# Kernel tuning notes

Measured on AMD Instinct MI355X. Metric: run time of the kernel, lower is better.

The kernel has to match this reference:

```python
import jax, jax.numpy as jnp
import numpy as np

B, T, D_MODEL, HEAD = 4, 4096, 1024, 64

def setup_inputs() -> dict:
    key = jax.random.key(0)
    ks = jax.random.split(key, 7)
    s = 0.02  # typical init scale
    return {
        "x":  jax.random.normal(ks[0], (B, T, D_MODEL), dtype=jnp.float32),
        "Wq": jax.random.normal(ks[1], (D_MODEL, HEAD), dtype=jnp.float32) * s,
        "bq": jnp.zeros((HEAD,), dtype=jnp.float32),
        "Wk": jax.random.normal(ks[2], (D_MODEL, HEAD), dtype=jnp.float32) * s,
        "bk": jnp.zeros((HEAD,), dtype=jnp.float32),
        "Wv": jax.random.normal(ks[3], (D_MODEL, HEAD), dtype=jnp.float32) * s,
        "bv": jnp.zeros((HEAD,), dtype=jnp.float32),
    }

def reference(x, Wq, bq, Wk, bk, Wv, bv):
    Bz, Tz, C = x.shape
    q = x @ Wq + bq                      # (B,T,H)
    k = x @ Wk + bk                      # (B,T,H)
    v = x @ Wv + bv                      # (B,T,H)
    # NOTE: original scales by sqrt(C) = sqrt(d_model), not sqrt(head_size)
    att = jnp.einsum("bth,bsh->bts", q, k) / jnp.sqrt(jnp.float32(C))
    causal = jnp.tril(jnp.ones((Tz, Tz), dtype=bool))
    att = jnp.where(causal, att, -jnp.inf)
    att = jax.nn.softmax(att, axis=-1)
    return jnp.einsum("bts,bsh->bth", att, v)  # (B,T,H)
```

## Files before the change

kernel.cpp:

```cpp
#include <hip/hip_runtime.h>
#include <hip/hip_bf16.h>
#include <hip/hip_fp16.h>

#define T_SEQ 4096
#define DMODEL 1024
#define HEAD 64
#define NBATCH 4
#define NSEG 544
#define S2LOG 0.04508422f

typedef __attribute__((ext_vector_type(8))) short bf16x8;
typedef __attribute__((ext_vector_type(4))) float f32x4;

__device__ __forceinline__ unsigned short f2bf(float f) {
    unsigned int b = __float_as_uint(f);
    unsigned int r = b + 0x7FFFu + ((b >> 16) & 1u);
    return (unsigned short)(r >> 16);
}
__device__ __forceinline__ unsigned int pk_bf16(float a, float b) {
    __hip_bfloat162 h = __float22bfloat162_rn(make_float2(a, b));
    unsigned int u; __builtin_memcpy(&u, &h, 4); return u;
}
__device__ __forceinline__ void dma16(const void* g, void* s) {
    __builtin_amdgcn_global_load_lds(
        (const __attribute__((address_space(1))) unsigned int*)g,
        (__attribute__((address_space(3))) unsigned int*)s, 16, 0, 0);
}

__global__ __launch_bounds__(256) void prep_w(
    const float* __restrict__ Wq, const float* __restrict__ Wk,
    const float* __restrict__ Wv, unsigned short* __restrict__ Wtb)
{
    __shared__ unsigned short tl[64 * 72];
    const int bid = blockIdx.x;
    const int m   = bid >> 4;
    const int k0  = (bid & 15) * 64;
    const float* W = (m == 0) ? Wq : (m == 1) ? Wk : Wv;
    const int t  = threadIdx.x;
    const int kr = t >> 2, qtr = t & 3;
#pragma unroll
    for (int i = 0; i < 4; ++i) {
        float4 wv4 = *(const float4*)&W[(k0 + kr) * 64 + qtr * 16 + i * 4];
        tl[(qtr * 16 + i * 4 + 0) * 72 + kr] = f2bf(wv4.x);
        tl[(qtr * 16 + i * 4 + 1) * 72 + kr] = f2bf(wv4.y);
        tl[(qtr * 16 + i * 4 + 2) * 72 + kr] = f2bf(wv4.z);
        tl[(qtr * 16 + i * 4 + 3) * 72 + kr] = f2bf(wv4.w);
    }
    __syncthreads();
#pragma unroll
    for (int c = 0; c < 2; ++c) {
        const int lin = c * 256 + t;
        const int n = lin >> 3, k8 = lin & 7;
        const int k = k0 + k8 * 8;
        const int sg = k >> 7, koff = k & 127;
        *(uint4*)&Wtb[((long)(sg * 192 + m * 64 + n)) * 128 + koff] =
            *(const uint4*)&tl[n * 72 + k8 * 8];
    }
}

__global__ __launch_bounds__(512, 2) void qkv_mfma(
    const float* __restrict__ x, const unsigned short* __restrict__ Wtb,
    const float* __restrict__ bq, const float* __restrict__ bk,
    const float* __restrict__ bv,
    unsigned short* __restrict__ qo, unsigned short* __restrict__ ko,
    unsigned short* __restrict__ vt)
{
    __shared__ __align__(16) unsigned short xs[2][8192];
    __shared__ __align__(16) unsigned short wsd[2][24576];
    const int t    = threadIdx.x;
    const int lane = t & 63;
    const int l15  = lane & 15, quad = lane >> 4;
    const int wv   = __builtin_amdgcn_readfirstlane(t >> 6);
    const int rowg = wv >> 2;
    const int colg = wv & 3;
    const long row0 = (long)blockIdx.x * 64;

    float bias[3];
#pragma unroll
    for (int ntl = 0; ntl < 3; ++ntl) {
        const int c = colg * 48 + ntl * 16 + l15;
        bias[ntl] = (c < 64) ? bq[c] : (c < 128) ? bk[c - 64] : bv[c - 128];
    }
    f32x4 acc[2][3];
#pragma unroll
    for (int mt = 0; mt < 2; ++mt)
#pragma unroll
        for (int ntl = 0; ntl < 3; ++ntl)
            acc[mt][ntl] = (f32x4){bias[ntl], bias[ntl], bias[ntl], bias[ntl]};

    float4 g[4];
    auto load_stage = [&](int sg) {
#pragma unroll
        for (int s = 0; s < 4; ++s) {
            const int id = s * 512 + t, row = id >> 5, off = id & 31;
            g[s] = *(const float4*)&x[(row0 + row) * DMODEL + sg * 128 + off * 4];
        }
    };
    auto write_stage = [&](int buf) {
#pragma unroll
        for (int s = 0; s < 4; ++s) {
            const int id = s * 512 + t, row = id >> 5, off = id & 31;
            uint2 u;
            u.x = pk_bf16(g[s].x, g[s].y);
            u.y = pk_bf16(g[s].z, g[s].w);
            *(uint2*)&xs[buf][row * 128 + ((off >> 1) ^ (row & 7)) * 8 + (off & 1) * 4] = u;
        }
    };
    auto dma_w = [&](int sg, int buf) {
#pragma unroll
        for (int j = 0; j < 6; ++j) {
            const int slot0 = (wv * 6 + j) * 64;
            const int slot  = slot0 + lane;
            const int col   = slot >> 4, ch = slot & 15;
            dma16(Wtb + ((long)(sg * 192 + col)) * 128 + ((ch ^ (col & 7)) * 8),
                  &wsd[buf][slot0 * 8]);
        }
    };

    load_stage(0);
    dma_w(0, 0);
    write_stage(0);

    for (int sg = 0; sg < 8; ++sg) {
        __syncthreads();
        if (sg + 1 < 8) {
            load_stage(sg + 1);
            dma_w(sg + 1, (sg + 1) & 1);
        }
        bf16x8 wf[3][4];
#pragma unroll
        for (int ntl = 0; ntl < 3; ++ntl)
#pragma unroll
            for (int kq = 0; kq < 4; ++kq) {
                const int col = colg * 48 + ntl * 16 + l15;
                wf[ntl][kq] = *(const bf16x8*)&wsd[sg & 1][col * 128
                                                           + (((kq * 4 + quad) ^ (col & 7))) * 8];
            }
#pragma unroll
        for (int mt = 0; mt < 2; ++mt)
#pragma unroll
            for (int kq = 0; kq < 4; ++kq) {
                const int row = rowg * 32 + mt * 16 + l15;
                bf16x8 a = *(const bf16x8*)&xs[sg & 1][row * 128
                                                       + ((kq * 4 + quad) ^ (row & 7)) * 8];
#pragma unroll
                for (int ntl = 0; ntl < 3; ++ntl)
                    acc[mt][ntl] = __builtin_amdgcn_mfma_f32_16x16x32_bf16(a, wf[ntl][kq], acc[mt][ntl], 0, 0, 0);
            }
        if (sg + 1 < 8) write_stage((sg + 1) & 1);
    }
#pragma unroll
    for (int mt = 0; mt < 2; ++mt)
#pragma unroll
        for (int ntl = 0; ntl < 3; ++ntl) {
            const int c = colg * 48 + ntl * 16 + l15;
            const long tr0 = row0 + rowg * 32 + mt * 16 + quad * 4;
            if (c < 64) {
#pragma unroll
                for (int r = 0; r < 4; ++r)
                    qo[(tr0 + r) * HEAD + c] = f2bf(acc[mt][ntl][r] * S2LOG);
            } else if (c < 128) {
#pragma unroll
                for (int r = 0; r < 4; ++r)
                    ko[(tr0 + r) * HEAD + (c - 64)] = f2bf(acc[mt][ntl][r]);
            } else {
                const int b = (int)(tr0 >> 12), tloc = (int)(tr0 & 4095);
                uint2 pv;
                pv.x = pk_bf16(acc[mt][ntl][0], acc[mt][ntl][1]);
                pv.y = pk_bf16(acc[mt][ntl][2], acc[mt][ntl][3]);
                *(uint2*)&vt[((long)(b * HEAD + (c - 128))) * T_SEQ + tloc] = pv;
            }
        }
}

__global__ __launch_bounds__(256, 3) void flash_seg(
    const unsigned short* __restrict__ qg,
    const unsigned short* __restrict__ kg,
    const unsigned short* __restrict__ vtg,
    __half* __restrict__ opart, float* __restrict__ ml)
{
    __shared__ __align__(16) unsigned short kv_s[2][8192];
    __shared__ __align__(16) unsigned short p_s[4][16 * 72];
    const int t0   = threadIdx.x;
    const int lane = t0 & 63;
    const int l15  = lane & 15, quad = lane >> 4;
    const int wv   = __builtin_amdgcn_readfirstlane(t0 >> 6);

    const int bid = (int)blockIdx.x;
    const int sid = (NSEG - 1) - (bid >> 2);
    const int b   = bid & 3;

    int kk = 0, pref = 0;
#pragma unroll
    for (int i = 0; i < 15; ++i) {
        const int cnt = 4 * (kk + 1);
        if (sid >= pref + cnt) { pref += cnt; ++kk; }
    }
    const int S   = kk + 1;
    const int rem = sid - pref;
    const int t   = kk * 4 + rem / S;
    const int si  = rem % S;
    const int r0  = t * 64;
    const int rw  = r0 + wv * 16;
    const int nck = t + 1;
    const int c0  = (si * nck) / S, c1 = ((si + 1) * nck) / S;
    const long bbase = (long)b * T_SEQ;
    const int gidx = b * NSEG + sid;

    bf16x8 qf[2];
#pragma unroll
    for (int h = 0; h < 2; ++h)
        qf[h] = *(const bf16x8*)&qg[(bbase + rw + l15) * HEAD + h * 32 + quad * 8];

    f32x4 o[4];
#pragma unroll
    for (int dt = 0; dt < 4; ++dt) o[dt] = (f32x4){0.f, 0.f, 0.f, 0.f};
    float lrun = 0.f;
    unsigned short* ps = p_s[wv];

    auto dma_chunk = [&](int key0, int buf) {
#pragma unroll
        for (int i = 0; i < 2; ++i) {
            const int jj  = wv * 2 + i;
            const int kl  = jj * 8 + (lane >> 3);
            const int dlg = (lane & 7) ^ ((lane >> 3) & 7);
            dma16(kg + (bbase + key0 + kl) * HEAD + dlg * 8,
                  &kv_s[buf][jj * 512]);
        }
#pragma unroll
        for (int i = 0; i < 2; ++i) {
            const int jj  = wv * 2 + i;
            const int dim = jj * 8 + (lane >> 3);
            const int klg = (lane & 7) ^ ((lane >> 3) & 7);
            dma16(vtg + ((long)(b * HEAD + dim)) * T_SEQ + key0 + klg * 8,
                  &kv_s[buf][4096 + jj * 512]);
        }
    };
    dma_chunk(c0 * 64, 0);

    for (int c = c0; c < c1; ++c) {
        const int key0 = c * 64;
        const int cur  = (c - c0) & 1;
        __syncthreads();
        if (c + 1 < c1) dma_chunk((c + 1) * 64, cur ^ 1);

        f32x4 st[4];
#pragma unroll
        for (int mt = 0; mt < 4; ++mt) {
            const int key_l = mt * 16 + l15;
            bf16x8 k0 = *(const bf16x8*)&kv_s[cur][key_l * 64 + ((quad    ) ^ (l15 & 7)) * 8];
            bf16x8 k1 = *(const bf16x8*)&kv_s[cur][key_l * 64 + ((quad + 4) ^ (l15 & 7)) * 8];
            f32x4 z = (f32x4){0.f, 0.f, 0.f, 0.f};
            z = __builtin_amdgcn_mfma_f32_16x16x32_bf16(k0, qf[0], z, 0, 0, 0);
            st[mt] = __builtin_amdgcn_mfma_f32_16x16x32_bf16(k1, qf[1], st[mt] = z, 0, 0, 0);
        }
        bf16x8 vf[4][2];
#pragma unroll
        for (int dt = 0; dt < 4; ++dt) {
            const int dim = dt * 16 + l15;
            vf[dt][0] = *(const bf16x8*)&kv_s[cur][4096 + dim * 64 + ((quad    ) ^ (l15 & 7)) * 8];
            vf[dt][1] = *(const bf16x8*)&kv_s[cur][4096 + dim * 64 + ((quad + 4) ^ (l15 & 7)) * 8];
        }
        if (key0 + 63 > rw) {
            const int row = rw + l15;
#pragma unroll
            for (int mt = 0; mt < 4; ++mt)
#pragma unroll
                for (int r = 0; r < 4; ++r) {
                    const int key = key0 + mt * 16 + quad * 4 + r;
                    st[mt][r] = (key <= row) ? st[mt][r] : -30000.f;
                }
        }
        float psum = 0.f;
#pragma unroll
        for (int mt = 0; mt < 4; ++mt) {
            float e0 = exp2f(st[mt][0]), e1 = exp2f(st[mt][1]);
            float e2 = exp2f(st[mt][2]), e3 = exp2f(st[mt][3]);
            psum += (e0 + e1) + (e2 + e3);
            *(unsigned int*)&ps[l15 * 72 + mt * 16 + quad * 4]     = pk_bf16(e0, e1);
            *(unsigned int*)&ps[l15 * 72 + mt * 16 + quad * 4 + 2] = pk_bf16(e2, e3);
        }
        psum += __shfl_xor(psum, 16);
        psum += __shfl_xor(psum, 32);
        lrun += psum;
        __builtin_amdgcn_wave_barrier();
        bf16x8 pf[2];
#pragma unroll
        for (int g = 0; g < 2; ++g)
            pf[g] = *(const bf16x8*)&ps[l15 * 72 + g * 32 + quad * 8];
        __builtin_amdgcn_wave_barrier();
#pragma unroll
        for (int dt = 0; dt < 4; ++dt) {
            o[dt] = __builtin_amdgcn_mfma_f32_16x16x32_bf16(vf[dt][0], pf[0], o[dt], 0, 0, 0);
            o[dt] = __builtin_amdgcn_mfma_f32_16x16x32_bf16(vf[dt][1], pf[1], o[dt], 0, 0, 0);
        }
    }

    const float inv = (lrun > 0.f) ? 1.f / lrun : 0.f;
    __half* op = opart + (long)gidx * 4096;
#pragma unroll
    for (int dt = 0; dt < 4; ++dt) {
        __half2 h0 = __floats2half2_rn(o[dt][0] * inv, o[dt][1] * inv);
        __half2 h1 = __floats2half2_rn(o[dt][2] * inv, o[dt][3] * inv);
        uint2 u; __builtin_memcpy(&u.x, &h0, 4); __builtin_memcpy(&u.y, &h1, 4);
        *(uint2*)&op[(wv * 16 + l15) * HEAD + dt * 16 + quad * 4] = u;
    }
    if (quad == 0)
        ml[(long)gidx * 64 + wv * 16 + l15] = lrun;
}

__global__ __launch_bounds__(256) void merge_seg(
    const __half* __restrict__ opart, const float* __restrict__ ml,
    float* __restrict__ out)
{
    const int bid = blockIdx.x;
    const int half = bid & 1, t = (bid >> 1) & 63, b = bid >> 7;
    const int kk = t >> 2, S = kk + 1;
    const int base_sid = 2 * kk * (kk + 1) + (t & 3) * S;
    const int tid = threadIdx.x;
    const int row = half * 32 + (tid >> 3), col0 = (tid & 7) * 8;

    float acc[8];
#pragma unroll
    for (int j = 0; j < 8; ++j) acc[j] = 0.f;
    float L = 0.f;
    for (int si = 0; si < S; ++si) {
        const long g = (long)(b * NSEG + base_sid + si);
        const float l = ml[g * 64 + row];
        L += l;
        const __half* op = opart + g * 4096 + row * 64 + col0;
        uint4 u = *(const uint4*)op;
        __half2 h01, h23, h45, h67;
        __builtin_memcpy(&h01, &u.x, 4); __builtin_memcpy(&h23, &u.y, 4);
        __builtin_memcpy(&h45, &u.z, 4); __builtin_memcpy(&h67, &u.w, 4);
        float2 f01 = __half22float2(h01), f23 = __half22float2(h23);
        float2 f45 = __half22float2(h45), f67 = __half22float2(h67);
        acc[0] += l * f01.x; acc[1] += l * f01.y;
        acc[2] += l * f23.x; acc[3] += l * f23.y;
        acc[4] += l * f45.x; acc[5] += l * f45.y;
        acc[6] += l * f67.x; acc[7] += l * f67.y;
    }
    const float inv = 1.f / L;
    float* dst = out + ((long)(b * T_SEQ + t * 64 + row)) * HEAD + col0;
#pragma unroll
    for (int h = 0; h < 2; ++h) {
        float4 ov = {acc[h * 4] * inv, acc[h * 4 + 1] * inv,
                     acc[h * 4 + 2] * inv, acc[h * 4 + 3] * inv};
        *(float4*)(dst + h * 4) = ov;
    }
}

extern "C" void kernel_launch(void* const* d_in, const int* in_sizes, int n_in,
                              void* d_out, int out_size, void* d_ws, size_t ws_size,
                              hipStream_t stream) {
    const float* x  = (const float*)d_in[0];
    const float* Wq = (const float*)d_in[1];
    const float* bq = (const float*)d_in[2];
    const float* Wk = (const float*)d_in[3];
    const float* bk = (const float*)d_in[4];
    const float* Wv = (const float*)d_in[5];
    const float* bv = (const float*)d_in[6];
    float* outp = (float*)d_out;

    char* wsb = (char*)d_ws;
    unsigned short* wtb = (unsigned short*)(wsb);
    unsigned short* qw  = (unsigned short*)(wsb + 393216);
    unsigned short* kw  = (unsigned short*)(wsb + 2490368);
    unsigned short* vtw = (unsigned short*)(wsb + 4587520);
    __half* opart       = (__half*)(wsb + 6684672);
    float*  mlp         = (float*)(wsb + 24510464);

    prep_w<<<dim3(48), dim3(256), 0, stream>>>(Wq, Wk, Wv, wtb);
    qkv_mfma<<<dim3(256), dim3(512), 0, stream>>>(
        x, wtb, bq, bk, bv, qw, kw, vtw);
    flash_seg<<<dim3(NSEG * NBATCH), dim3(256), 0, stream>>>(qw, kw, vtw, opart, mlp);
    merge_seg<<<dim3(512), dim3(256), 0, stream>>>(opart, mlp, outp);
}
```

Baseline: 147.0 us.

## Split flash tile work 2x2 across waves by query half and key half

Each of the four waves in the flash kernel now handles 32 query rows against 32 keys of each chunk, instead of 16 query rows against all 64 keys. Each K fragment loaded from LDS is reused across two query groups, and each wave reads only half of V, so per-wave LDS reads and the P staging buffer shrink. After the loop, the two key-half waves reduce their partial outputs and row sums through LDS, adding extra syncs and an fp32 exchange buffer, and the causal mask check becomes finer-grained per key half.

```diff
diff --git a/kernel.cpp b/kernel.cpp
--- a/kernel.cpp
+++ b/kernel.cpp
@@ -180,11 +180,14 @@
     __half* __restrict__ opart, float* __restrict__ ml)
 {
     __shared__ __align__(16) unsigned short kv_s[2][8192];
-    __shared__ __align__(16) unsigned short p_s[4][16 * 72];
+    __shared__ __align__(16) unsigned short p_s[4][32 * 40];
+    __shared__ __align__(16) float l_lds[2][32];
     const int t0   = threadIdx.x;
     const int lane = t0 & 63;
     const int l15  = lane & 15, quad = lane >> 4;
     const int wv   = __builtin_amdgcn_readfirstlane(t0 >> 6);
+    const int qh   = wv & 1;
+    const int kh2  = wv >> 1;
 
     const int bid = (int)blockIdx.x;
     const int sid = (NSEG - 1) - (bid >> 2);
@@ -201,21 +204,26 @@
     const int t   = kk * 4 + rem / S;
     const int si  = rem % S;
     const int r0  = t * 64;
-    const int rw  = r0 + wv * 16;
+    const int rw  = r0 + qh * 32;
     const int nck = t + 1;
     const int c0  = (si * nck) / S, c1 = ((si + 1) * nck) / S;
     const long bbase = (long)b * T_SEQ;
     const int gidx = b * NSEG + sid;
 
-    bf16x8 qf[2];
-#pragma unroll
-    for (int h = 0; h < 2; ++h)
-        qf[h] = *(const bf16x8*)&qg[(bbase + rw + l15) * HEAD + h * 32 + quad * 8];
-
-    f32x4 o[4];
-#pragma unroll
-    for (int dt = 0; dt < 4; ++dt) o[dt] = (f32x4){0.f, 0.f, 0.f, 0.f};
-    float lrun = 0.f;
+    bf16x8 qf[2][2];
+#pragma unroll
+    for (int cg = 0; cg < 2; ++cg)
+#pragma unroll
+        for (int h = 0; h < 2; ++h)
+            qf[cg][h] = *(const bf16x8*)&qg[(bbase + rw + cg * 16 + l15) * HEAD
+                                            + h * 32 + quad * 8];
+
+    f32x4 o[4][2];
+#pragma unroll
+    for (int dt = 0; dt < 4; ++dt)
+#pragma unroll
+        for (int cg = 0; cg < 2; ++cg) o[dt][cg] = (f32x4){0.f, 0.f, 0.f, 0.f};
+    float lrun[2] = {0.f, 0.f};
     unsigned short* ps = p_s[wv];
 
     auto dma_chunk = [&](int key0, int buf) {
@@ -244,69 +252,114 @@
         __syncthreads();
         if (c + 1 < c1) dma_chunk((c + 1) * 64, cur ^ 1);
 
-        f32x4 st[4];
-#pragma unroll
-        for (int mt = 0; mt < 4; ++mt) {
-            const int key_l = mt * 16 + l15;
-            bf16x8 k0 = *(const bf16x8*)&kv_s[cur][key_l * 64 + ((quad    ) ^ (l15 & 7)) * 8];
-            bf16x8 k1 = *(const bf16x8*)&kv_s[cur][key_l * 64 + ((quad + 4) ^ (l15 & 7)) * 8];
-            f32x4 z = (f32x4){0.f, 0.f, 0.f, 0.f};
-            z = __builtin_amdgcn_mfma_f32_16x16x32_bf16(k0, qf[0], z, 0, 0, 0);
-            st[mt] = __builtin_amdgcn_mfma_f32_16x16x32_bf16(k1, qf[1], st[mt] = z, 0, 0, 0);
-        }
-        bf16x8 vf[4][2];
+        bf16x8 kf[2][2];
+#pragma unroll
+        for (int mt = 0; mt < 2; ++mt)
+#pragma unroll
+            for (int kd = 0; kd < 2; ++kd) {
+                const int key_l = kh2 * 32 + mt * 16 + l15;
+                kf[mt][kd] = *(const bf16x8*)&kv_s[cur][key_l * 64
+                                                        + ((kd * 4 + quad) ^ (l15 & 7)) * 8];
+            }
+        f32x4 st[2][2];
+#pragma unroll
+        for (int mt = 0; mt < 2; ++mt)
+#pragma unroll
+            for (int cg = 0; cg < 2; ++cg) {
+                f32x4 z = (f32x4){0.f, 0.f, 0.f, 0.f};
+                z = __builtin_amdgcn_mfma_f32_16x16x32_bf16(kf[mt][0], qf[cg][0], z, 0, 0, 0);
+                st[mt][cg] = __builtin_amdgcn_mfma_f32_16x16x32_bf16(kf[mt][1], qf[cg][1], z, 0, 0, 0);
+            }
+        bf16x8 vf[4];
 #pragma unroll
         for (int dt = 0; dt < 4; ++dt) {
             const int dim = dt * 16 + l15;
-            vf[dt][0] = *(const bf16x8*)&kv_s[cur][4096 + dim * 64 + ((quad    ) ^ (l15 & 7)) * 8];
-            vf[dt][1] = *(const bf16x8*)&kv_s[cur][4096 + dim * 64 + ((quad + 4) ^ (l15 & 7)) * 8];
-        }
-        if (key0 + 63 > rw) {
-            const int row = rw + l15;
-#pragma unroll
-            for (int mt = 0; mt < 4; ++mt)
-#pragma unroll
-                for (int r = 0; r < 4; ++r) {
-                    const int key = key0 + mt * 16 + quad * 4 + r;
-                    st[mt][r] = (key <= row) ? st[mt][r] : -30000.f;
-                }
-        }
-        float psum = 0.f;
-#pragma unroll
-        for (int mt = 0; mt < 4; ++mt) {
-            float e0 = exp2f(st[mt][0]), e1 = exp2f(st[mt][1]);
-            float e2 = exp2f(st[mt][2]), e3 = exp2f(st[mt][3]);
-            psum += (e0 + e1) + (e2 + e3);
-            *(unsigned int*)&ps[l15 * 72 + mt * 16 + quad * 4]     = pk_bf16(e0, e1);
-            *(unsigned int*)&ps[l15 * 72 + mt * 16 + quad * 4 + 2] = pk_bf16(e2, e3);
-        }
-        psum += __shfl_xor(psum, 16);
-        psum += __shfl_xor(psum, 32);
-        lrun += psum;
+            vf[dt] = *(const bf16x8*)&kv_s[cur][4096 + dim * 64
+                                                 + ((kh2 * 4 + quad) ^ (l15 & 7)) * 8];
+        }
+        if (key0 + kh2 * 32 + 31 > rw) {
+#pragma unroll
+            for (int mt = 0; mt < 2; ++mt)
+#pragma unroll
+                for (int cg = 0; cg < 2; ++cg)
+#pragma unroll
+                    for (int r = 0; r < 4; ++r) {
+                        const int key = key0 + kh2 * 32 + mt * 16 + quad * 4 + r;
+                        const int row = rw + cg * 16 + l15;
+                        st[mt][cg][r] = (key <= row) ? st[mt][cg][r] : -30000.f;
+                    }
+        }
+        float psum[2] = {0.f, 0.f};
+#pragma unroll
+        for (int mt = 0; mt < 2; ++mt)
+#pragma unroll
+            for (int cg = 0; cg < 2; ++cg) {
+                float e0 = exp2f(st[mt][cg][0]), e1 = exp2f(st[mt][cg][1]);
+                float e2 = exp2f(st[mt][cg][2]), e3 = exp2f(st[mt][cg][3]);
+                psum[cg] += (e0 + e1) + (e2 + e3);
+                *(unsigned int*)&ps[(cg * 16 + l15) * 40 + mt * 16 + quad * 4]     = pk_bf16(e0, e1);
+                *(unsigned int*)&ps[(cg * 16 + l15) * 40 + mt * 16 + quad * 4 + 2] = pk_bf16(e2, e3);
+            }
+#pragma unroll
+        for (int cg = 0; cg < 2; ++cg) {
+            psum[cg] += __shfl_xor(psum[cg], 16);
+            psum[cg] += __shfl_xor(psum[cg], 32);
+            lrun[cg] += psum[cg];
+        }
         __builtin_amdgcn_wave_barrier();
         bf16x8 pf[2];
 #pragma unroll
-        for (int g = 0; g < 2; ++g)
-            pf[g] = *(const bf16x8*)&ps[l15 * 72 + g * 32 + quad * 8];
+        for (int cg = 0; cg < 2; ++cg)
+            pf[cg] = *(const bf16x8*)&ps[(cg * 16 + l15) * 40 + quad * 8];
         __builtin_amdgcn_wave_barrier();
 #pragma unroll
-        for (int dt = 0; dt < 4; ++dt) {
-            o[dt] = __builtin_amdgcn_mfma_f32_16x16x32_bf16(vf[dt][0], pf[0], o[dt], 0, 0, 0);
-            o[dt] = __builtin_amdgcn_mfma_f32_16x16x32_bf16(vf[dt][1], pf[1], o[dt], 0, 0, 0);
-        }
-    }
-
-    const float inv = (lrun > 0.f) ? 1.f / lrun : 0.f;
-    __half* op = opart + (long)gidx * 4096;
-#pragma unroll
-    for (int dt = 0; dt < 4; ++dt) {
-        __half2 h0 = __floats2half2_rn(o[dt][0] * inv, o[dt][1] * inv);
-        __half2 h1 = __floats2half2_rn(o[dt][2] * inv, o[dt][3] * inv);
-        uint2 u; __builtin_memcpy(&u.x, &h0, 4); __builtin_memcpy(&u.y, &h1, 4);
-        *(uint2*)&op[(wv * 16 + l15) * HEAD + dt * 16 + quad * 4] = u;
-    }
-    if (quad == 0)
-        ml[(long)gidx * 64 + wv * 16 + l15] = lrun;
+        for (int dt = 0; dt < 4; ++dt)
+#pragma unroll
+            for (int cg = 0; cg < 2; ++cg)
+                o[dt][cg] = __builtin_amdgcn_mfma_f32_16x16x32_bf16(vf[dt], pf[cg], o[dt][cg], 0, 0, 0);
+    }
+
+    __syncthreads();
+    float* o_lds = (float*)&kv_s[0][0];
+    if (kh2 == 1) {
+#pragma unroll
+        for (int dt = 0; dt < 4; ++dt)
+#pragma unroll
+            for (int cg = 0; cg < 2; ++cg)
+                *(f32x4*)&o_lds[(qh * 32 + cg * 16 + l15) * 68 + dt * 16 + quad * 4] = o[dt][cg];
+        if (quad == 0) {
+#pragma unroll
+            for (int cg = 0; cg < 2; ++cg)
+                l_lds[qh][cg * 16 + l15] = lrun[cg];
+        }
+    }
+    __syncthreads();
+    if (kh2 == 0) {
+        float inv[2];
+#pragma unroll
+        for (int cg = 0; cg < 2; ++cg) {
+            lrun[cg] += l_lds[qh][cg * 16 + l15];
+            inv[cg] = (lrun[cg] > 0.f) ? 1.f / lrun[cg] : 0.f;
+        }
+        __half* op = opart + (long)gidx * 4096;
+#pragma unroll
+        for (int dt = 0; dt < 4; ++dt)
+#pragma unroll
+            for (int cg = 0; cg < 2; ++cg) {
+                f32x4 ov = o[dt][cg];
+                f32x4 add = *(const f32x4*)&o_lds[(qh * 32 + cg * 16 + l15) * 68 + dt * 16 + quad * 4];
+                ov += add;
+                __half2 h0 = __floats2half2_rn(ov[0] * inv[cg], ov[1] * inv[cg]);
+                __half2 h1 = __floats2half2_rn(ov[2] * inv[cg], ov[3] * inv[cg]);
+                uint2 u; __builtin_memcpy(&u.x, &h0, 4); __builtin_memcpy(&u.y, &h1, 4);
+                *(uint2*)&op[(qh * 32 + cg * 16 + l15) * HEAD + dt * 16 + quad * 4] = u;
+            }
+        if (quad == 0) {
+#pragma unroll
+            for (int cg = 0; cg < 2; ++cg)
+                ml[(long)gidx * 64 + qh * 32 + cg * 16 + l15] = lrun[cg];
+        }
+    }
 }
 
 __global__ __launch_bounds__(256) void merge_seg(
```

Measured after the change: 148.5 us. Within noise of the previous version (+1.1%).
